# Performance work log

Hardware: AMD Instinct MI355X
Metric: run time of the kernel (lower is better)

Reference implementation:

```python
import jax, jax.numpy as jnp
import numpy as np

B = 32768   # batch
F = 32      # per-node feature dim
H = 256     # hidden width
M = 4       # modules per node
OUT = 8     # final output dim
INIT_W = 0.003
B_INIT = 0.1


def _lin(k, din, dout):
    # fanin_init-style uniform weights, bias filled with 0.1 (hidden layers)
    s = 1.0 / np.sqrt(din)
    W = jax.random.uniform(k, (M, din, dout), jnp.float32, -s, s)
    b = jnp.full((M, dout), B_INIT, jnp.float32)
    return W, b


def setup_inputs() -> dict:
    key = jax.random.key(0)
    ks = jax.random.split(key, 16)
    feats = jax.random.normal(ks[0], (B, 4 * F), jnp.float32)
    idx = jax.random.randint(ks[1], (B, 4), 0, M)
    onehots = jax.nn.one_hot(idx, M, dtype=jnp.float32).reshape(B, 4 * M)
    input_val = jnp.concatenate([feats, onehots], axis=1)  # [B,144]

    W00, b00 = _lin(ks[2], F, H)        # node0 post layer 0
    W01, b01 = _lin(ks[3], H, H)        # node0 post layer 1
    Wpre1, bpre1 = _lin(ks[4], F, H)    # node1 pre
    Wpost1, bpost1 = _lin(ks[5], 2 * H, H)  # node1 interface (prev 256 + own 256)
    Wpre2, bpre2 = _lin(ks[6], F, H)
    Wpost2, bpost2 = _lin(ks[7], 2 * H, H)
    Wpre3, bpre3 = _lin(ks[8], F, H)
    Wpost3, bpost3 = _lin(ks[9], 2 * H, H)
    # final output layer: uniform(-init_w, init_w) for W and b, identity act
    Wfin3 = jax.random.uniform(ks[10], (M, H, OUT), jnp.float32, -INIT_W, INIT_W)
    bfin3 = jax.random.uniform(ks[11], (M, OUT), jnp.float32, -INIT_W, INIT_W)
    return dict(input_val=input_val,
                W00=W00, b00=b00, W01=W01, b01=b01,
                Wpre1=Wpre1, bpre1=bpre1, Wpost1=Wpost1, bpost1=bpost1,
                Wpre2=Wpre2, bpre2=bpre2, Wpost2=Wpost2, bpost2=bpost2,
                Wpre3=Wpre3, bpre3=bpre3, Wpost3=Wpost3, bpost3=bpost3,
                Wfin3=Wfin3, bfin3=bfin3)


def _select(h, onehot):
    # per-row pick of the assigned module's output: [B,M,D],[B,M] -> [B,D]
    return jnp.einsum('bmo,bm->bo', h, onehot)


def reference(input_val, W00, b00, W01, b01,
              Wpre1, bpre1, Wpost1, bpost1,
              Wpre2, bpre2, Wpost2, bpost2,
              Wpre3, bpre3, Wpost3, bpost3,
              Wfin3, bfin3):
    feat = lambda j: input_val[:, j * F:(j + 1) * F]
    oh = lambda j: input_val[:, 4 * F + j * M: 4 * F + (j + 1) * M]

    # node 0: two hidden layers, module-dispatched (dense-all-modules + one-hot combine)
    h = jax.nn.relu(jnp.einsum('bi,mio->bmo', feat(0), W00) + b00)
    h = jax.nn.relu(jnp.einsum('bmi,mio->bmo', h, W01) + b01)
    x = _select(h, oh(0))  # [B,H]

    def node(x_prev, fj, ohj, Wpre, bpre, Wpost, bpost):
        hp = jax.nn.relu(jnp.einsum('bi,mio->bmo', fj, Wpre) + bpre)
        # interface layer consumes concat([x_prev, hp]); split the weight to
        # avoid materializing [B,M,2H]
        hq = jax.nn.relu(jnp.einsum('bi,mio->bmo', x_prev, Wpost[:, :H, :])
                         + jnp.einsum('bmi,mio->bmo', hp, Wpost[:, H:, :])
                         + bpost)
        return hq  # [B,M,H]

    x = _select(node(x, feat(1), oh(1), Wpre1, bpre1, Wpost1, bpost1), oh(1))
    x = _select(node(x, feat(2), oh(2), Wpre2, bpre2, Wpost2, bpost2), oh(2))

    h3 = node(x, feat(3), oh(3), Wpre3, bpre3, Wpost3, bpost3)  # [B,M,H]
    out = jnp.einsum('bmi,mio->bmo', h3, Wfin3) + bfin3          # final linear, identity act
    return _select(out, oh(3))  # [B,OUT]
```

## Files before the change

### kernel.cpp

```cpp
#include <hip/hip_runtime.h>

#define NB 32768
#define MAXTILE 768
#define ROWS 64
#define NT 4

typedef short s8v __attribute__((ext_vector_type(8)));
typedef short s4v __attribute__((ext_vector_type(4)));
typedef float f4v __attribute__((ext_vector_type(4)));
typedef unsigned short u16;
typedef unsigned short u16x4 __attribute__((ext_vector_type(4)));
typedef unsigned int u32;
typedef unsigned char u8;

__device__ __forceinline__ float bf2f(u16 u) { return __uint_as_float(((u32)u) << 16); }
__device__ __forceinline__ u16 f2bf(float f) {
    u32 x = __float_as_uint(f);
    x += 0x7FFFu + ((x >> 16) & 1u);
    return (u16)(x >> 16);
}
__device__ __forceinline__ s8v ld8(const u16* p) { return *reinterpret_cast<const s8v*>(p); }

#define MFMA16(a, b, c) __builtin_amdgcn_mfma_f32_16x16x32_bf16((a), (b), (c), 0, 0, 0)

__device__ __forceinline__ void detect_flag(const void* input, int tid, int* shflag)
{
    if (tid < 64) {
        u32 w = ((const u32*)input)[tid];
        u32 h0 = w & 0xFFFFu;
        u32 e0 = (h0 >> 7) & 0xFFu;
        bool plaus = (h0 == 0u) || (e0 >= 96u && e0 <= 143u);
        unsigned long long m = __ballot(plaus);
        if (tid == 0) *shflag = (__popcll(m) >= 48) ? 1 : 0;
    }
}

struct RepArgs {
    const void* W01; const void* Wp[3]; const void* pre[4]; const void* fin;
    const void* bias[9];
    u16 *rPre, *rW01, *rWp[3], *rFin, *cbias;
};

__global__ __launch_bounds__(256) void prepA_kernel(const void* __restrict__ inputv,
                                                    int* __restrict__ gcnt,
                                                    int* __restrict__ perm2,
                                                    u16* __restrict__ feats16,
                                                    RepArgs R)
{
    __shared__ int lcnt[256];
    __shared__ int sBase[256];
    __shared__ u16 T[8192];
    __shared__ int shmisc;
    int tid = threadIdx.x;
    int b = blockIdx.x;
    detect_flag(inputv, tid, &shmisc);
    __syncthreads();
    int flag = shmisc;

    if (b < 128) {
        lcnt[tid] = 0;
        __syncthreads();
        int row = (b << 8) + tid;
        const u32* in32 = (const u32*)inputv;
        const u16* in16 = (const u16*)inputv;
        int key = 0;
        if (flag) {
#pragma unroll
            for (int j = 0; j < 4; j++) {
                u16x4 v = *(const u16x4*)(in16 + row * 144 + 128 + j * 4);
                int m = v[1] ? 1 : (v[2] ? 2 : (v[3] ? 3 : 0));
                key |= m << (j << 1);
            }
        } else {
#pragma unroll
            for (int j = 0; j < 4; j++) {
                const u32* p = in32 + row * 144 + 128 + j * 4;
                u32 v1 = p[1], v2 = p[2], v3 = p[3];
                int m = v1 ? 1 : (v2 ? 2 : (v3 ? 3 : 0));
                key |= m << (j << 1);
            }
        }
        int loc = atomicAdd(&lcnt[key], 1);
        __syncthreads();
        int c = lcnt[tid];
        sBase[tid] = c ? atomicAdd(&gcnt[tid], c) : 0;
        __syncthreads();
        int slot = sBase[key] + loc;
        if (slot < 512) perm2[(key << 9) + slot] = row;

        int r0 = b << 8;
        if (flag) {
            for (int i = tid; i < 256 * 16; i += 256) {
                int r = r0 + (i >> 4), j = (i & 15) << 3;
                *(s8v*)(feats16 + ((size_t)r << 7) + j) = ld8(in16 + (size_t)r * 144 + j);
            }
        } else {
            for (int i = tid; i < 256 * 32; i += 256) {
                int r = r0 + (i >> 5), j = (i & 31) << 2;
                f4v f = *(const f4v*)(in32 + (size_t)r * 144 + j);
                s4v p;
#pragma unroll
                for (int q = 0; q < 4; q++) p[q] = (short)f2bf(f[q]);
                *(s4v*)(feats16 + ((size_t)r << 7) + j) = p;
            }
        }
        return;
    }

    int rb = b - 128;
    const void* src = nullptr; u16* dst = nullptr; int K = 0, k0 = 0, mrow = 0;
    if (rb < 32) {
        int m = rb >> 3, s = rb & 7;
        src = R.W01; dst = R.rW01 + (m * 8 + s) * 8192; K = 256; k0 = s * 32; mrow = m;
    } else if (rb < 224) {
        int idx = rb - 32, mat = idx >> 6, r = idx & 63, m = r >> 4, s = r & 15;
        src = R.Wp[mat]; dst = R.rWp[mat] + (m * 16 + s) * 8192; K = 512; k0 = s * 32; mrow = m;
    } else if (rb < 240) {
        int idx = rb - 224, mat = idx >> 2, m = idx & 3;
        src = R.pre[mat]; dst = R.rPre + (mat * 4 + m) * 8192; K = 32; k0 = 0; mrow = m;
    } else if (rb < 244) {
        int m = rb - 240;
        const u16* s16 = (const u16*)R.fin;
        const float* s32 = (const float*)R.fin;
        for (int i = tid; i < 2048; i += 256) {
            int si = (m * 256 + (i >> 3)) * 8 + (i & 7);
            T[i] = flag ? s16[si] : f2bf(s32[si]);
        }
        __syncthreads();
        u16* d = R.rFin + m * 4096;
        for (int i = tid; i < 4096; i += 256) {
            int s = i >> 9, lane = (i >> 3) & 63, j = i & 7;
            int q = lane >> 4, l16 = lane & 15;
            int k = s * 32 + q * 8 + j;
            d[i] = (l16 < 8) ? T[k * 8 + l16] : (u16)0;
        }
        return;
    } else {
        const int sz[9] = {1024,1024,1024,1024,1024,1024,1024,1024,32};
        const int of[9] = {0,1024,2048,3072,4096,5120,6144,7168,8192};
        for (int i = tid; i < 8224; i += 256) {
            int t = i, e = 0;
            while (t >= sz[e]) { t -= sz[e]; e++; }
            R.cbias[of[e] + t] = flag ? ((const u16*)R.bias[e])[t]
                                      : f2bf(((const float*)R.bias[e])[t]);
        }
        return;
    }
    const u16* s16 = (const u16*)src;
    const float* s32 = (const float*)src;
    for (int i = tid; i < 8192; i += 256) {
        int k = i >> 8, n = i & 255;
        int srcIdx = (mrow * K + k0 + k) * 256 + n;
        T[i] = flag ? s16[srcIdx] : f2bf(s32[srcIdx]);
    }
    __syncthreads();
    for (int i = tid; i < 8192; i += 256) {
        int mt = i >> 9, lane = (i >> 3) & 63, j = i & 7;
        int k = ((lane >> 4) << 3) + j, n = (mt << 4) + (lane & 15);
        dst[i] = T[(k << 8) + n];
    }
}

struct MainP { const u16 *rPre, *rW01, *rWp1, *rWp2, *rWp3, *rFin, *cbias, *feats; };

__global__ __launch_bounds__(512, 6) void main_kernel(
    const void* __restrict__ inRaw,
    const int* __restrict__ gcnt, const int* __restrict__ perm2,
    MainP P, void* __restrict__ outp)
{
    __shared__ __align__(16) u16 xhB[16384];
    __shared__ int rowids[ROWS];
    __shared__ int shflag;
    __shared__ int sMeta[4];

    int tid = threadIdx.x;
    int lane = tid & 63, w = tid >> 6, quad = lane >> 4, l16 = lane & 15;

    int b = blockIdx.x;
    int t = ((b & 7) * (MAXTILE / 8)) + (b >> 3);

    detect_flag(inRaw, tid, &shflag);

    if (tid < 64) {
        int4 g = *(const int4*)(gcnt + tid * 4);
        int tot4[4] = {g.x, g.y, g.z, g.w};
        int tiles4[4], lsum = 0;
#pragma unroll
        for (int j = 0; j < 4; j++) { tiles4[j] = (tot4[j] + 63) >> 6; lsum += tiles4[j]; }
        int pre = lsum;
#pragma unroll
        for (int off = 1; off < 64; off <<= 1) {
            int v = __shfl_up(pre, off, 64);
            if (tid >= off) pre += v;
        }
        int run = pre - lsum;
#pragma unroll
        for (int j = 0; j < 4; j++) {
            if (t >= run && t < run + tiles4[j]) {
                sMeta[0] = tid * 4 + j;
                sMeta[1] = t - run;
                sMeta[2] = tot4[j];
            }
            run += tiles4[j];
        }
        if (tid == 63) sMeta[3] = pre;
    }
    __syncthreads();
    if (t >= sMeta[3]) return;
    int key = sMeta[0], tau = sMeta[1], tot = sMeta[2];
    int cntIn = tot - tau * ROWS; if (cntIn > ROWS) cntIn = ROWS;
    if (tid < ROWS) {
        int g = tid < cntIn ? tid : cntIn - 1;
        rowids[tid] = perm2[(key << 9) + tau * ROWS + g];
    }
    __syncthreads();

    int flag = shflag;
    int rows_[NT];
#pragma unroll
    for (int nt = 0; nt < NT; nt++) rows_[nt] = rowids[nt * 16 + l16];

    const u16* feats = P.feats;
    int mt0 = w << 1, mt1 = mt0 + 1;
    int stA = ((quad >> 1) * 16 + l16) * 8 + (quad & 1) * 4;

    f4v acc0[NT], acc1[NT];

    auto gemm_run = [&](const u16* Ab) {
        const u16* base0 = Ab + mt0 * 512 + lane * 8;
        const u16* base1 = Ab + mt1 * 512 + lane * 8;
        s8v A0[2], A1[2];
        A0[0] = ld8(base0);        A1[0] = ld8(base1);
        A0[1] = ld8(base0 + 8192); A1[1] = ld8(base1 + 8192);
        __builtin_amdgcn_s_setprio(1);
#pragma unroll
        for (int s = 0; s < 8; s++) {
            s8v c0 = A0[s & 1], c1 = A1[s & 1];
            if (s + 2 < 8) {
                A0[s & 1] = ld8(base0 + (s + 2) * 8192);
                A1[s & 1] = ld8(base1 + (s + 2) * 8192);
            }
#pragma unroll
            for (int nt = 0; nt < NT; nt++) {
                s8v B = ld8(&xhB[((nt * 8 + s) << 9) + lane * 8]);
                acc0[nt] = MFMA16(c0, B, acc0[nt]);
                acc1[nt] = MFMA16(c1, B, acc1[nt]);
            }
        }
        __builtin_amdgcn_s_setprio(0);
    };

    for (int node = 0; node < 4; node++) {
        int m = (key >> (node << 1)) & 3;

        {
            u16x4 b0 = *(const u16x4*)(P.cbias + node * 2048 + 1024 + m * 256 + mt0 * 16 + quad * 4);
            u16x4 b1 = *(const u16x4*)(P.cbias + node * 2048 + 1024 + m * 256 + mt1 * 16 + quad * 4);
            f4v f0, f1;
#pragma unroll
            for (int r = 0; r < 4; r++) { f0[r] = bf2f(b0[r]); f1[r] = bf2f(b1[r]); }
#pragma unroll
            for (int nt = 0; nt < NT; nt++) { acc0[nt] = f0; acc1[nt] = f1; }
        }

        const u16* wb2;
        if (node > 0) {
            const u16* WB = (node == 1 ? P.rWp1 : (node == 2 ? P.rWp2 : P.rWp3)) + m * 16 * 8192;
            gemm_run(WB);
            __syncthreads();
            wb2 = WB + 8 * 8192;
        } else {
            wb2 = P.rW01 + m * 8 * 8192;
        }

        {
            s8v fb[NT];
#pragma unroll
            for (int nt = 0; nt < NT; nt++)
                fb[nt] = ld8(feats + ((size_t)rows_[nt] << 7) + (node << 5) + (quad << 3));
            const u16* preB = P.rPre + ((node << 2) + m) * 8192;
#pragma unroll
            for (int ci = 0; ci < 2; ci++) {
                int mt = mt0 + ci;
                s8v a = ld8(preB + mt * 512 + lane * 8);
                u16x4 bv = *(const u16x4*)(P.cbias + node * 2048 + m * 256 + mt * 16 + quad * 4);
                f4v bias;
#pragma unroll
                for (int r = 0; r < 4; r++) bias[r] = bf2f(bv[r]);
#pragma unroll
                for (int nt = 0; nt < NT; nt++) {
                    f4v c = MFMA16(a, fb[nt], bias);
                    s4v p;
#pragma unroll
                    for (int r = 0; r < 4; r++) { float v = c[r] > 0.f ? c[r] : 0.f; p[r] = (short)f2bf(v); }
                    *(s4v*)&xhB[((nt * 8 + w) << 9) + ci * 256 + stA] = p;
                }
            }
        }
        __syncthreads();

        gemm_run(wb2);
        __syncthreads();

#pragma unroll
        for (int ci = 0; ci < 2; ci++) {
#pragma unroll
            for (int nt = 0; nt < NT; nt++) {
                f4v a = ci ? acc1[nt] : acc0[nt];
                s4v p;
#pragma unroll
                for (int r = 0; r < 4; r++) { float v = a[r] > 0.f ? a[r] : 0.f; p[r] = (short)f2bf(v); }
                *(s4v*)&xhB[((nt * 8 + w) << 9) + ci * 256 + stA] = p;
            }
        }
        __syncthreads();
    }

    if (w < NT) {
        int m3 = (key >> 6) & 3;
        f4v c;
#pragma unroll
        for (int r = 0; r < 4; r++)
            c[r] = (quad < 2) ? bf2f(P.cbias[8192 + m3 * 8 + quad * 4 + r]) : 0.f;
#pragma unroll
        for (int s = 0; s < 8; s++) {
            s8v A = ld8(P.rFin + m3 * 4096 + s * 512 + lane * 8);
            s8v B = ld8(&xhB[((w * 8 + s) << 9) + lane * 8]);
            c = MFMA16(A, B, c);
        }
        int bidx = w * 16 + l16;
        if (quad < 2 && bidx < cntIn) {
            int row = rowids[bidx];
            if (flag) {
                s4v p;
#pragma unroll
                for (int r = 0; r < 4; r++) p[r] = (short)f2bf(c[r]);
                *(s4v*)((u16*)outp + row * 8 + quad * 4) = p;
            } else {
                *(f4v*)((float*)outp + row * 8 + quad * 4) = c;
            }
        }
    }
}

extern "C" void kernel_launch(void* const* d_in, const int* in_sizes, int n_in,
                              void* d_out, int out_size, void* d_ws, size_t ws_size,
                              hipStream_t stream)
{
    (void)in_sizes; (void)n_in; (void)out_size;
    const void* input  = d_in[0];
    const void* W00    = d_in[1];
    const void* b00    = d_in[2];
    const void* W01    = d_in[3];
    const void* b01    = d_in[4];
    const void* Wpre1  = d_in[5];
    const void* bpre1  = d_in[6];
    const void* Wpost1 = d_in[7];
    const void* bpost1 = d_in[8];
    const void* Wpre2  = d_in[9];
    const void* bpre2  = d_in[10];
    const void* Wpost2 = d_in[11];
    const void* bpost2 = d_in[12];
    const void* Wpre3  = d_in[13];
    const void* bpre3  = d_in[14];
    const void* Wpost3 = d_in[15];
    const void* bpost3 = d_in[16];
    const void* Wfin   = d_in[17];
    const void* bfin   = d_in[18];

    char* base = (char*)d_ws;
    size_t off = 0;
    auto alloc = [&](size_t bytes) -> char* {
        char* p = base + off;
        off += (bytes + 255) & ~(size_t)255;
        return p;
    };
    int*  gcnt      = (int*)alloc(256 * 4);
    int*  perm2     = (int*)alloc(256 * 512 * 4);
    u16*  feats16   = (u16*)alloc((size_t)NB * 128 * 2);
    u16*  cbias    = (u16*)alloc(8224 * 2);
    u16*  rPre     = (u16*)alloc(131072 * 2);
    u16*  rW01     = (u16*)alloc(262144 * 2);
    u16*  rWp1     = (u16*)alloc(524288 * 2);
    u16*  rWp2     = (u16*)alloc(524288 * 2);
    u16*  rWp3     = (u16*)alloc(524288 * 2);
    u16*  rFin     = (u16*)alloc(16384 * 2);
    if (off > ws_size) return;

    RepArgs R;
    R.W01 = W01; R.Wp[0] = Wpost1; R.Wp[1] = Wpost2; R.Wp[2] = Wpost3;
    R.pre[0] = W00; R.pre[1] = Wpre1; R.pre[2] = Wpre2; R.pre[3] = Wpre3;
    R.fin = Wfin;
    R.bias[0] = b00;   R.bias[1] = b01;
    R.bias[2] = bpre1; R.bias[3] = bpost1;
    R.bias[4] = bpre2; R.bias[5] = bpost2;
    R.bias[6] = bpre3; R.bias[7] = bpost3;
    R.bias[8] = bfin;
    R.rPre = rPre; R.rW01 = rW01;
    R.rWp[0] = rWp1; R.rWp[1] = rWp2; R.rWp[2] = rWp3;
    R.rFin = rFin; R.cbias = cbias;

    hipMemsetAsync(gcnt, 0, 256 * 4, stream);
    prepA_kernel<<<373, 256, 0, stream>>>(input, gcnt, perm2, feats16, R);

    MainP P;
    P.rPre = rPre; P.rW01 = rW01; P.rWp1 = rWp1; P.rWp2 = rWp2; P.rWp3 = rWp3;
    P.rFin = rFin; P.cbias = cbias; P.feats = feats16;
    main_kernel<<<MAXTILE, 512, 0, stream>>>(input, gcnt, perm2, P, d_out);
}
```

Before: 204.7 us.

## Shrink row tiles to 32 and give each wave four output column tiles

```diff
diff --git a/kernel.cpp b/kernel.cpp
--- a/kernel.cpp
+++ b/kernel.cpp
@@ -1,9 +1,9 @@
 #include <hip/hip_runtime.h>
 
 #define NB 32768
-#define MAXTILE 768
-#define ROWS 64
-#define NT 4
+#define MAXTILE 1280
+#define ROWS 32
+#define NT 2
 
 typedef short s8v __attribute__((ext_vector_type(8)));
 typedef short s4v __attribute__((ext_vector_type(4)));
@@ -163,12 +163,12 @@
 
 struct MainP { const u16 *rPre, *rW01, *rWp1, *rWp2, *rWp3, *rFin, *cbias, *feats; };
 
-__global__ __launch_bounds__(512, 6) void main_kernel(
+__global__ __launch_bounds__(256, 5) void main_kernel(
     const void* __restrict__ inRaw,
     const int* __restrict__ gcnt, const int* __restrict__ perm2,
     MainP P, void* __restrict__ outp)
 {
-    __shared__ __align__(16) u16 xhB[16384];
+    __shared__ __align__(16) u16 xhB[8192];
     __shared__ int rowids[ROWS];
     __shared__ int shflag;
     __shared__ int sMeta[4];
@@ -186,7 +186,7 @@
         int tot4[4] = {g.x, g.y, g.z, g.w};
         int tiles4[4], lsum = 0;
 #pragma unroll
-        for (int j = 0; j < 4; j++) { tiles4[j] = (tot4[j] + 63) >> 6; lsum += tiles4[j]; }
+        for (int j = 0; j < 4; j++) { tiles4[j] = (tot4[j] + 31) >> 5; lsum += tiles4[j]; }
         int pre = lsum;
 #pragma unroll
         for (int off = 1; off < 64; off <<= 1) {
@@ -221,31 +221,37 @@
     for (int nt = 0; nt < NT; nt++) rows_[nt] = rowids[nt * 16 + l16];
 
     const u16* feats = P.feats;
-    int mt0 = w << 1, mt1 = mt0 + 1;
     int stA = ((quad >> 1) * 16 + l16) * 8 + (quad & 1) * 4;
 
-    f4v acc0[NT], acc1[NT];
+    f4v acc[4][NT];
 
     auto gemm_run = [&](const u16* Ab) {
-        const u16* base0 = Ab + mt0 * 512 + lane * 8;
-        const u16* base1 = Ab + mt1 * 512 + lane * 8;
-        s8v A0[2], A1[2];
-        A0[0] = ld8(base0);        A1[0] = ld8(base1);
-        A0[1] = ld8(base0 + 8192); A1[1] = ld8(base1 + 8192);
+        const u16* base = Ab + (w * 4) * 512 + lane * 8;
+        s8v A[2][4];
+#pragma unroll
+        for (int ci = 0; ci < 4; ci++) {
+            A[0][ci] = ld8(base + ci * 512);
+            A[1][ci] = ld8(base + 8192 + ci * 512);
+        }
         __builtin_amdgcn_s_setprio(1);
 #pragma unroll
         for (int s = 0; s < 8; s++) {
-            s8v c0 = A0[s & 1], c1 = A1[s & 1];
+            s8v B0 = ld8(&xhB[((0 * 8 + s) << 9) + lane * 8]);
+            s8v B1 = ld8(&xhB[((1 * 8 + s) << 9) + lane * 8]);
+            s8v c0 = A[s & 1][0], c1 = A[s & 1][1], c2 = A[s & 1][2], c3 = A[s & 1][3];
             if (s + 2 < 8) {
-                A0[s & 1] = ld8(base0 + (s + 2) * 8192);
-                A1[s & 1] = ld8(base1 + (s + 2) * 8192);
-            }
-#pragma unroll
-            for (int nt = 0; nt < NT; nt++) {
-                s8v B = ld8(&xhB[((nt * 8 + s) << 9) + lane * 8]);
-                acc0[nt] = MFMA16(c0, B, acc0[nt]);
-                acc1[nt] = MFMA16(c1, B, acc1[nt]);
-            }
+#pragma unroll
+                for (int ci = 0; ci < 4; ci++)
+                    A[s & 1][ci] = ld8(base + (s + 2) * 8192 + ci * 512);
+            }
+            acc[0][0] = MFMA16(c0, B0, acc[0][0]);
+            acc[0][1] = MFMA16(c0, B1, acc[0][1]);
+            acc[1][0] = MFMA16(c1, B0, acc[1][0]);
+            acc[1][1] = MFMA16(c1, B1, acc[1][1]);
+            acc[2][0] = MFMA16(c2, B0, acc[2][0]);
+            acc[2][1] = MFMA16(c2, B1, acc[2][1]);
+            acc[3][0] = MFMA16(c3, B0, acc[3][0]);
+            acc[3][1] = MFMA16(c3, B1, acc[3][1]);
         }
         __builtin_amdgcn_s_setprio(0);
     };
@@ -253,14 +259,13 @@
     for (int node = 0; node < 4; node++) {
         int m = (key >> (node << 1)) & 3;
 
-        {
-            u16x4 b0 = *(const u16x4*)(P.cbias + node * 2048 + 1024 + m * 256 + mt0 * 16 + quad * 4);
-            u16x4 b1 = *(const u16x4*)(P.cbias + node * 2048 + 1024 + m * 256 + mt1 * 16 + quad * 4);
-            f4v f0, f1;
-#pragma unroll
-            for (int r = 0; r < 4; r++) { f0[r] = bf2f(b0[r]); f1[r] = bf2f(b1[r]); }
-#pragma unroll
-            for (int nt = 0; nt < NT; nt++) { acc0[nt] = f0; acc1[nt] = f1; }
+#pragma unroll
+        for (int ci = 0; ci < 4; ci++) {
+            u16x4 bv = *(const u16x4*)(P.cbias + node * 2048 + 1024 + m * 256 + (w * 4 + ci) * 16 + quad * 4);
+            f4v f;
+#pragma unroll
+            for (int r = 0; r < 4; r++) f[r] = bf2f(bv[r]);
+            acc[ci][0] = f; acc[ci][1] = f;
         }
 
         const u16* wb2;
@@ -274,26 +279,24 @@
         }
 
         {
-            s8v fb[NT];
-#pragma unroll
-            for (int nt = 0; nt < NT; nt++)
-                fb[nt] = ld8(feats + ((size_t)rows_[nt] << 7) + (node << 5) + (quad << 3));
-            const u16* preB = P.rPre + ((node << 2) + m) * 8192;
-#pragma unroll
-            for (int ci = 0; ci < 2; ci++) {
-                int mt = mt0 + ci;
-                s8v a = ld8(preB + mt * 512 + lane * 8);
-                u16x4 bv = *(const u16x4*)(P.cbias + node * 2048 + m * 256 + mt * 16 + quad * 4);
+            s8v fb0 = ld8(feats + ((size_t)rows_[0] << 7) + (node << 5) + (quad << 3));
+            s8v fb1 = ld8(feats + ((size_t)rows_[1] << 7) + (node << 5) + (quad << 3));
+            const u16* preB = P.rPre + ((node << 2) + m) * 8192 + (w * 4) * 512 + lane * 8;
+#pragma unroll
+            for (int ci = 0; ci < 4; ci++) {
+                s8v a = ld8(preB + ci * 512);
+                u16x4 bv = *(const u16x4*)(P.cbias + node * 2048 + m * 256 + (w * 4 + ci) * 16 + quad * 4);
                 f4v bias;
 #pragma unroll
                 for (int r = 0; r < 4; r++) bias[r] = bf2f(bv[r]);
+                int sb = 2 * w + (ci >> 1), sub = (ci & 1) << 8;
 #pragma unroll
                 for (int nt = 0; nt < NT; nt++) {
-                    f4v c = MFMA16(a, fb[nt], bias);
+                    f4v c = MFMA16(a, nt ? fb1 : fb0, bias);
                     s4v p;
 #pragma unroll
                     for (int r = 0; r < 4; r++) { float v = c[r] > 0.f ? c[r] : 0.f; p[r] = (short)f2bf(v); }
-                    *(s4v*)&xhB[((nt * 8 + w) << 9) + ci * 256 + stA] = p;
+                    *(s4v*)&xhB[((nt * 8 + sb) << 9) + sub + stA] = p;
                 }
             }
         }
@@ -303,14 +306,15 @@
         __syncthreads();
 
 #pragma unroll
-        for (int ci = 0; ci < 2; ci++) {
+        for (int ci = 0; ci < 4; ci++) {
+            int sb = 2 * w + (ci >> 1), sub = (ci & 1) << 8;
 #pragma unroll
             for (int nt = 0; nt < NT; nt++) {
-                f4v a = ci ? acc1[nt] : acc0[nt];
+                f4v a = acc[ci][nt];
                 s4v p;
 #pragma unroll
                 for (int r = 0; r < 4; r++) { float v = a[r] > 0.f ? a[r] : 0.f; p[r] = (short)f2bf(v); }
-                *(s4v*)&xhB[((nt * 8 + w) << 9) + ci * 256 + stA] = p;
+                *(s4v*)&xhB[((nt * 8 + sb) << 9) + sub + stA] = p;
             }
         }
         __syncthreads();
@@ -406,5 +410,5 @@
     MainP P;
     P.rPre = rPre; P.rW01 = rW01; P.rWp1 = rWp1; P.rWp2 = rWp2; P.rWp3 = rWp3;
     P.rFin = rFin; P.cbias = cbias; P.feats = feats16;
-    main_kernel<<<MAXTILE, 512, 0, stream>>>(input, gcnt, perm2, P, d_out);
+    main_kernel<<<MAXTILE, 256, 0, stream>>>(input, gcnt, perm2, P, d_out);
 }
```

Result: faster. 196.2 us (-4.2%).
